# Optimization experiments

Measured on AMD Instinct MI355X. Metric: run time of the kernel, lower is better.

## Reference

```python
import jax, jax.numpy as jnp
import numpy as np

N_NODES = 50000
N_EDGES = 600000
IN_F = 128
HID_F = 128
OUT_F = 128


def setup_inputs() -> dict:
    key = jax.random.key(0)
    ks = jax.random.split(key, 12)
    features = jax.random.normal(ks[0], (N_NODES, IN_F), dtype=jnp.float32)
    src = jax.random.randint(ks[1], (N_EDGES,), 0, N_NODES, dtype=jnp.int32)
    dst = jax.random.randint(ks[2], (N_EDGES,), 0, N_NODES, dtype=jnp.int32)

    def lin(k, fan_in, fan_out):
        s = 1.0 / jnp.sqrt(fan_in)
        return jax.random.uniform(k, (fan_in, fan_out), jnp.float32, -s, s)

    return {
        "features": features, "src": src, "dst": dst,
        "W1_self": lin(ks[3], IN_F, HID_F), "W1_neigh": lin(ks[4], IN_F, HID_F),
        "b1": jnp.zeros((HID_F,), jnp.float32),
        "W2_self": lin(ks[5], HID_F, HID_F), "W2_neigh": lin(ks[6], HID_F, HID_F),
        "b2": jnp.zeros((HID_F,), jnp.float32),
        "W3_self": lin(ks[7], HID_F, OUT_F), "W3_neigh": lin(ks[8], HID_F, OUT_F),
        "b3": jnp.zeros((OUT_F,), jnp.float32),
    }


def _sage_mean(x, src, dst, W_self, W_neigh, b):
    # gather source-node features along edges, mean-reduce into dst nodes
    msgs = x[src]                                                # [E, d]
    summed = jax.ops.segment_sum(msgs, dst, num_segments=N_NODES)  # [N, d]
    deg = jax.ops.segment_sum(jnp.ones((dst.shape[0],), x.dtype), dst,
                              num_segments=N_NODES)               # [N]
    mean = summed / jnp.maximum(deg, 1.0)[:, None]
    return x @ W_self + mean @ W_neigh + b


def reference(features, src, dst,
              W1_self, W1_neigh, b1,
              W2_self, W2_neigh, b2,
              W3_self, W3_neigh, b3):
    x = features.reshape(features.shape[0], -1)  # Flatten (no-op for 2D)
    x = jax.nn.relu(_sage_mean(x, src, dst, W1_self, W1_neigh, b1))
    x = jax.nn.relu(_sage_mean(x, src, dst, W2_self, W2_neigh, b2))
    x = _sage_mean(x, src, dst, W3_self, W3_neigh, b3)
    return x
```

## Files before the change

### kernel.cpp

```cpp
#include <hip/hip_runtime.h>

#define NN 50000
#define NE 600000
#define F 128

typedef __attribute__((ext_vector_type(4))) float f4;
typedef __attribute__((ext_vector_type(4))) float f32x4;
typedef __bf16 bf16x8 __attribute__((ext_vector_type(8)));
typedef short short8v __attribute__((ext_vector_type(8)));
typedef unsigned short u16x8 __attribute__((ext_vector_type(8)));

__device__ inline ushort f2bf(float f) {
    uint u = __builtin_bit_cast(uint, f);
    uint r = (u + 0x7FFFu + ((u >> 16) & 1u)) >> 16;
    return (ushort)r;
}
__device__ inline float bf2f(ushort u) {
    uint t = ((uint)u) << 16;
    return __builtin_bit_cast(float, t);
}


__global__ void count_deg(const int* __restrict__ dst, int* __restrict__ deg, int E) {
    int e = blockIdx.x * blockDim.x + threadIdx.x;
    if (e < E) atomicAdd(&deg[dst[e]], 1);
}

__global__ __launch_bounds__(1024) void scan_part1(const int* __restrict__ deg,
                                                   int* __restrict__ bsum, int N) {
    __shared__ int ws[16];
    int tid = threadIdx.x;
    int idx = blockIdx.x * 1024 + tid;
    int v = (idx < N) ? deg[idx] : 0;
    #pragma unroll
    for (int o = 32; o; o >>= 1) v += __shfl_down(v, o);
    if ((tid & 63) == 0) ws[tid >> 6] = v;
    __syncthreads();
    if (tid < 64) {
        int t = (tid < 16) ? ws[tid] : 0;
        #pragma unroll
        for (int o = 8; o; o >>= 1) t += __shfl_down(t, o);
        if (tid == 0) bsum[blockIdx.x] = t;
    }
}

__global__ __launch_bounds__(1024) void scan_part3(const int* __restrict__ deg,
                                                   const int* __restrict__ bsum,
                                                   int* __restrict__ off,
                                                   int* __restrict__ cur,
                                                   float* __restrict__ recip,
                                                   int N, int NB) {
    __shared__ int wsum[16];
    __shared__ int sbase;
    int tid = threadIdx.x;
    int wid = tid >> 6;
    int lane = tid & 63;
    if (tid < 64) {
        int v = (tid < NB) ? bsum[tid] : 0;
        int x = v;
        #pragma unroll
        for (int o = 1; o < 64; o <<= 1) {
            int t = __shfl_up(x, o);
            if (lane >= o) x += t;
        }
        if (tid == blockIdx.x) sbase = x - v;
    }
    int idx = blockIdx.x * 1024 + tid;
    int v = (idx < N) ? deg[idx] : 0;
    int x = v;
    #pragma unroll
    for (int o = 1; o < 64; o <<= 1) {
        int t = __shfl_up(x, o);
        if (lane >= o) x += t;
    }
    if (lane == 63) wsum[wid] = x;
    __syncthreads();
    if (tid == 0) {
        int a = 0;
        #pragma unroll
        for (int w = 0; w < 16; ++w) { int t = wsum[w]; wsum[w] = a; a += t; }
    }
    __syncthreads();
    int incl = x + wsum[wid];
    if (idx < N) {
        int start = sbase + incl - v;
        off[idx] = start;
        cur[idx] = start;
        recip[idx] = 1.0f / (float)max(v, 1);
    }
}

__global__ void fill_csr(const int* __restrict__ src, const int* __restrict__ dst,
                         int* __restrict__ cur, int* __restrict__ csr, int E) {
    int e = blockIdx.x * blockDim.x + threadIdx.x;
    if (e < E) {
        int pos = atomicAdd(&cur[dst[e]], 1);
        csr[pos] = src[e];
    }
}


__global__ __launch_bounds__(256) void wt_prep(const float* __restrict__ W1s, const float* __restrict__ W1n,
                                               const float* __restrict__ W2s, const float* __restrict__ W2n,
                                               const float* __restrict__ W3s, const float* __restrict__ W3n,
                                               ushort* __restrict__ Bt1, ushort* __restrict__ Bt2,
                                               ushort* __restrict__ Bt3) {
    int layer = blockIdx.y;
    const float* Ws = (layer == 0) ? W1s : (layer == 1) ? W2s : W3s;
    const float* Wn = (layer == 0) ? W1n : (layer == 1) ? W2n : W3n;
    ushort* Bt = (layer == 0) ? Bt1 : (layer == 1) ? Bt2 : Bt3;
    int col = blockIdx.x;
    int k = threadIdx.x;
    float v = (k < 128) ? Ws[k * 128 + col] : Wn[(k - 128) * 128 + col];
    Bt[col * 256 + k] = f2bf(v);
}


__global__ __launch_bounds__(256) void to_bf16(const float* __restrict__ in,
                                               ushort* __restrict__ out, int n8) {
    int i = blockIdx.x * 256 + threadIdx.x;
    if (i < n8) {
        const f4* p = (const f4*)in + (size_t)i * 2;
        f4 a = p[0], b = p[1];
        short8v w;
        w[0] = (short)f2bf(a[0]); w[1] = (short)f2bf(a[1]);
        w[2] = (short)f2bf(a[2]); w[3] = (short)f2bf(a[3]);
        w[4] = (short)f2bf(b[0]); w[5] = (short)f2bf(b[1]);
        w[6] = (short)f2bf(b[2]); w[7] = (short)f2bf(b[3]);
        ((short8v*)out)[i] = w;
    }
}


template <int RELU, int OUTBF>
__global__ __launch_bounds__(256) void sage_layer(const ushort* __restrict__ xb,
                                                  const int* __restrict__ off,
                                                  const int* __restrict__ deg,
                                                  const float* __restrict__ recip,
                                                  const int* __restrict__ csr,
                                                  const ushort* __restrict__ Bt,
                                                  const float* __restrict__ bias,
                                                  void* __restrict__ outp, int N) {
    __shared__ ushort sa[32 * 256];
    int tid = threadIdx.x;
    int r0 = blockIdx.x * 32;

    {
        int row = tid >> 3;
        int c = tid & 7;
        int grow = r0 + row;
        uint sw = ((uint)row & 7u) << 4;
        uint base = (uint)(row * 512 + c * 32);
        short8v w0 = (short8v)0, w1 = (short8v)0;
        if (grow < N) {
            const short8v* sp = (const short8v*)&xb[(size_t)grow * 128 + c * 16];
            w0 = sp[0]; w1 = sp[1];
        }
        *(short8v*)((char*)sa + (base ^ sw)) = w0;
        *(short8v*)((char*)sa + ((base + 16) ^ sw)) = w1;
    }

    {
        int g = tid >> 4;
        int l16 = tid & 15;
        const ushort* xpb = xb + (size_t)l16 * 8;
        #pragma unroll
        for (int rep = 0; rep < 2; ++rep) {
            int row = g + rep * 16;
            int node = r0 + row;
            float a[8] = {0.f, 0.f, 0.f, 0.f, 0.f, 0.f, 0.f, 0.f};
            if (node < N) {
                int start = off[node];
                int d = deg[node];
                int nfull = d & ~7;
                int i = 0;
                for (; i < nfull; i += 8) {
                    int s[8];
                    #pragma unroll
                    for (int u = 0; u < 8; ++u) s[u] = csr[start + i + u];
                    u16x8 v[8];
                    #pragma unroll
                    for (int u = 0; u < 8; ++u) v[u] = *(const u16x8*)(xpb + (size_t)s[u] * 128);
                    #pragma unroll
                    for (int u = 0; u < 8; ++u) {
                        #pragma unroll
                        for (int j = 0; j < 8; ++j) a[j] += bf2f(v[u][j]);
                    }
                }
                if (i < d) {
                    int dm1 = d - 1;
                    int s[8];
                    #pragma unroll
                    for (int u = 0; u < 8; ++u) {
                        int idx = i + u;
                        s[u] = csr[start + ((idx < dm1) ? idx : dm1)];
                    }
                    u16x8 v[8];
                    #pragma unroll
                    for (int u = 0; u < 8; ++u) v[u] = *(const u16x8*)(xpb + (size_t)s[u] * 128);
                    #pragma unroll
                    for (int u = 0; u < 8; ++u) {
                        float m = (i + u < d) ? 1.f : 0.f;
                        #pragma unroll
                        for (int j = 0; j < 8; ++j) a[j] += m * bf2f(v[u][j]);
                    }
                }
                float r = recip[node];
                #pragma unroll
                for (int j = 0; j < 8; ++j) a[j] *= r;
            }
            short8v w;
            #pragma unroll
            for (int j = 0; j < 8; ++j) w[j] = (short)f2bf(a[j]);
            uint sw = ((uint)row & 7u) << 4;
            uint addr = (uint)(row * 512 + 256 + l16 * 16);
            *(short8v*)((char*)sa + (addr ^ sw)) = w;
        }
    }
    __syncthreads();

    int lane = tid & 63;
    int wid = tid >> 6;
    int wr = wid & 1;
    int wc = wid >> 1;
    int l15 = lane & 15;
    int lg = lane >> 4;

    int arow = wr * 16 + l15;
    uint abase = (uint)(arow * 512 + lg * 16);
    uint asw = ((uint)arow & 7u) << 4;
    bf16x8 a[8];
    #pragma unroll
    for (int ks = 0; ks < 8; ++ks) {
        a[ks] = *(const bf16x8*)((const char*)sa + ((abase + (uint)ks * 64) ^ asw));
    }

    f32x4 acc[4];
    #pragma unroll
    for (int ct = 0; ct < 4; ++ct) acc[ct] = (f32x4)0.f;

    #pragma unroll
    for (int ct = 0; ct < 4; ++ct) {
        int bcol = wc * 64 + ct * 16 + l15;
        const ushort* bp = Bt + bcol * 256 + lg * 8;
        #pragma unroll
        for (int ks = 0; ks < 8; ++ks) {
            bf16x8 b = *(const bf16x8*)(bp + ks * 32);
            acc[ct] = __builtin_amdgcn_mfma_f32_16x16x32_bf16(a[ks], b, acc[ct], 0, 0, 0);
        }
    }

    int crow = r0 + wr * 16 + lg * 4;
    #pragma unroll
    for (int ct = 0; ct < 4; ++ct) {
        int col = wc * 64 + ct * 16 + l15;
        float bv = bias[col];
        #pragma unroll
        for (int r = 0; r < 4; ++r) {
            int row = crow + r;
            if (row < N) {
                float v = acc[ct][r] + bv;
                if (RELU) v = fmaxf(v, 0.f);
                if (OUTBF) ((ushort*)outp)[(size_t)row * 128 + col] = f2bf(v);
                else       ((float*)outp)[(size_t)row * 128 + col] = v;
            }
        }
    }
}


extern "C" void kernel_launch(void* const* d_in, const int* in_sizes, int n_in,
                              void* d_out, int out_size, void* d_ws, size_t ws_size,
                              hipStream_t stream) {
    const float* feat = (const float*)d_in[0];
    const int* src = (const int*)d_in[1];
    const int* dst = (const int*)d_in[2];
    const float* W1s = (const float*)d_in[3];
    const float* W1n = (const float*)d_in[4];
    const float* b1 = (const float*)d_in[5];
    const float* W2s = (const float*)d_in[6];
    const float* W2n = (const float*)d_in[7];
    const float* b2 = (const float*)d_in[8];
    const float* W3s = (const float*)d_in[9];
    const float* W3n = (const float*)d_in[10];
    const float* b3 = (const float*)d_in[11];
    float* out = (float*)d_out;

    const int N = NN, E = NE;
    const int NB = (N + 1023) / 1024;

    char* p = (char*)d_ws;
    auto alloc = [&](size_t bytes) {
        char* q = p;
        p += (bytes + 255) & ~(size_t)255;
        return q;
    };
    int* deg = (int*)alloc((size_t)N * 4);
    int* off = (int*)alloc((size_t)N * 4);
    int* cur = (int*)alloc((size_t)N * 4);
    float* recip = (float*)alloc((size_t)N * 4);
    int* bsum = (int*)alloc(64 * 4);
    int* csr = (int*)alloc((size_t)E * 4);
    ushort* xb0 = (ushort*)alloc((size_t)N * F * 2);
    ushort* h1b = (ushort*)alloc((size_t)N * F * 2);
    ushort* h2b = (ushort*)alloc((size_t)N * F * 2);
    ushort* Bt1 = (ushort*)alloc(128 * 256 * 2);
    ushort* Bt2 = (ushort*)alloc(128 * 256 * 2);
    ushort* Bt3 = (ushort*)alloc(128 * 256 * 2);

    wt_prep<<<dim3(128, 3), 256, 0, stream>>>(W1s, W1n, W2s, W2n, W3s, W3n, Bt1, Bt2, Bt3);
    to_bf16<<<(N * F / 8 + 255) / 256, 256, 0, stream>>>(feat, xb0, N * F / 8);

    hipMemsetAsync(deg, 0, (size_t)N * 4, stream);
    count_deg<<<(E + 255) / 256, 256, 0, stream>>>(dst, deg, E);
    scan_part1<<<NB, 1024, 0, stream>>>(deg, bsum, N);
    scan_part3<<<NB, 1024, 0, stream>>>(deg, bsum, off, cur, recip, N, NB);
    fill_csr<<<(E + 255) / 256, 256, 0, stream>>>(src, dst, cur, csr, E);

    int grid = (N + 31) / 32;

    sage_layer<1, 1><<<grid, 256, 0, stream>>>(xb0, off, deg, recip, csr, Bt1, b1, h1b, N);
    sage_layer<1, 1><<<grid, 256, 0, stream>>>(h1b, off, deg, recip, csr, Bt2, b2, h2b, N);
    sage_layer<0, 0><<<grid, 256, 0, stream>>>(h2b, off, deg, recip, csr, Bt3, b3, out, N);
}
```

Measured before the change: 244.3 us.

## Halve rows per block and balance neighbor aggregation with shared atomic row queue

Each block now handles 16 node rows instead of 32, and the four 16-lane groups per wavefront pull rows dynamically from a shared atomic counter rather than being statically assigned two rows each. This is meant to even out work across groups when node degrees vary, and to give more blocks for occupancy and tail balance. The MFMA stage is re-split so each of the four waves computes 32 output columns over the 16 rows. The cost is an extra barrier and LDS atomics per row, a shuffle per row, and twice as many blocks, each reloading the weight matrix.

```diff
diff --git a/kernel.cpp b/kernel.cpp
--- a/kernel.cpp
+++ b/kernel.cpp
@@ -141,32 +141,34 @@
                                                   const ushort* __restrict__ Bt,
                                                   const float* __restrict__ bias,
                                                   void* __restrict__ outp, int N) {
-    __shared__ ushort sa[32 * 256];
+    __shared__ ushort sa[16 * 256];
+    __shared__ int wcnt;
     int tid = threadIdx.x;
-    int r0 = blockIdx.x * 32;
+    int r0 = blockIdx.x * 16;
+    if (tid == 0) wcnt = 0;
 
     {
-        int row = tid >> 3;
-        int c = tid & 7;
+        int row = tid >> 4;
+        int c = tid & 15;
         int grow = r0 + row;
         uint sw = ((uint)row & 7u) << 4;
-        uint base = (uint)(row * 512 + c * 32);
-        short8v w0 = (short8v)0, w1 = (short8v)0;
-        if (grow < N) {
-            const short8v* sp = (const short8v*)&xb[(size_t)grow * 128 + c * 16];
-            w0 = sp[0]; w1 = sp[1];
-        }
-        *(short8v*)((char*)sa + (base ^ sw)) = w0;
-        *(short8v*)((char*)sa + ((base + 16) ^ sw)) = w1;
-    }
+        uint base = (uint)(row * 512 + c * 16);
+        short8v w = (short8v)0;
+        if (grow < N) w = ((const short8v*)&xb[(size_t)grow * 128])[c];
+        *(short8v*)((char*)sa + (base ^ sw)) = w;
+    }
+    __syncthreads();
 
     {
-        int g = tid >> 4;
         int l16 = tid & 15;
+        int lanebase = (tid & 63) & ~15;
         const ushort* xpb = xb + (size_t)l16 * 8;
-        #pragma unroll
-        for (int rep = 0; rep < 2; ++rep) {
-            int row = g + rep * 16;
+        for (;;) {
+            int n = 0;
+            if (l16 == 0) n = atomicAdd(&wcnt, 1);
+            n = __shfl(n, lanebase);
+            if (n >= 16) break;
+            int row = n;
             int node = r0 + row;
             float a[8] = {0.f, 0.f, 0.f, 0.f, 0.f, 0.f, 0.f, 0.f};
             if (node < N) {
@@ -221,27 +223,24 @@
 
     int lane = tid & 63;
     int wid = tid >> 6;
-    int wr = wid & 1;
-    int wc = wid >> 1;
     int l15 = lane & 15;
     int lg = lane >> 4;
 
-    int arow = wr * 16 + l15;
-    uint abase = (uint)(arow * 512 + lg * 16);
-    uint asw = ((uint)arow & 7u) << 4;
+    uint abase = (uint)(l15 * 512 + lg * 16);
+    uint asw = ((uint)l15 & 7u) << 4;
     bf16x8 a[8];
     #pragma unroll
     for (int ks = 0; ks < 8; ++ks) {
         a[ks] = *(const bf16x8*)((const char*)sa + ((abase + (uint)ks * 64) ^ asw));
     }
 
-    f32x4 acc[4];
-    #pragma unroll
-    for (int ct = 0; ct < 4; ++ct) acc[ct] = (f32x4)0.f;
-
-    #pragma unroll
-    for (int ct = 0; ct < 4; ++ct) {
-        int bcol = wc * 64 + ct * 16 + l15;
+    f32x4 acc[2];
+    #pragma unroll
+    for (int ct = 0; ct < 2; ++ct) acc[ct] = (f32x4)0.f;
+
+    #pragma unroll
+    for (int ct = 0; ct < 2; ++ct) {
+        int bcol = wid * 32 + ct * 16 + l15;
         const ushort* bp = Bt + bcol * 256 + lg * 8;
         #pragma unroll
         for (int ks = 0; ks < 8; ++ks) {
@@ -250,10 +249,10 @@
         }
     }
 
-    int crow = r0 + wr * 16 + lg * 4;
-    #pragma unroll
-    for (int ct = 0; ct < 4; ++ct) {
-        int col = wc * 64 + ct * 16 + l15;
+    int crow = r0 + lg * 4;
+    #pragma unroll
+    for (int ct = 0; ct < 2; ++ct) {
+        int col = wid * 32 + ct * 16 + l15;
         float bv = bias[col];
         #pragma unroll
         for (int r = 0; r < 4; ++r) {
@@ -317,7 +316,7 @@
     scan_part3<<<NB, 1024, 0, stream>>>(deg, bsum, off, cur, recip, N, NB);
     fill_csr<<<(E + 255) / 256, 256, 0, stream>>>(src, dst, cur, csr, E);
 
-    int grid = (N + 31) / 32;
+    int grid = (N + 15) / 16;
 
     sage_layer<1, 1><<<grid, 256, 0, stream>>>(xb0, off, deg, recip, csr, Bt1, b1, h1b, N);
     sage_layer<1, 1><<<grid, 256, 0, stream>>>(h1b, off, deg, recip, csr, Bt2, b2, h2b, N);
```

Result: faster. 233.0 us, median of 2 (-4.6%).

## Dynamically assign aggregation rows via shared atomic counter and gather 16 neighbors per batch

Applied to the files above, without the earlier changes.

Replaces the static two-rows-per-16-lane-group assignment with a work queue: each 16-lane group grabs the next row index from a shared-memory atomic counter and broadcasts it by shuffle. This is meant to balance degree variance across groups within a block. It also merges the full and tail loops into one masked loop that issues 16 neighbor loads per iteration, raising memory-level parallelism. The cost is more registers, masked wasted loads for low-degree nodes (avg degree ~12), atomic traffic, and an added barrier.

```diff
diff --git a/kernel.cpp b/kernel.cpp
--- a/kernel.cpp
+++ b/kernel.cpp
@@ -142,8 +142,10 @@
                                                   const float* __restrict__ bias,
                                                   void* __restrict__ outp, int N) {
     __shared__ ushort sa[32 * 256];
+    __shared__ int wcnt;
     int tid = threadIdx.x;
     int r0 = blockIdx.x * 32;
+    if (tid == 0) wcnt = 0;
 
     {
         int row = tid >> 3;
@@ -159,48 +161,38 @@
         *(short8v*)((char*)sa + (base ^ sw)) = w0;
         *(short8v*)((char*)sa + ((base + 16) ^ sw)) = w1;
     }
+    __syncthreads();
 
     {
-        int g = tid >> 4;
         int l16 = tid & 15;
+        int lanebase = (tid & 63) & ~15;
         const ushort* xpb = xb + (size_t)l16 * 8;
-        #pragma unroll
-        for (int rep = 0; rep < 2; ++rep) {
-            int row = g + rep * 16;
+        for (;;) {
+            int n = 0;
+            if (l16 == 0) n = atomicAdd(&wcnt, 1);
+            n = __shfl(n, lanebase);
+            if (n >= 32) break;
+            int row = n;
             int node = r0 + row;
             float a[8] = {0.f, 0.f, 0.f, 0.f, 0.f, 0.f, 0.f, 0.f};
             if (node < N) {
                 int start = off[node];
                 int d = deg[node];
-                int nfull = d & ~7;
-                int i = 0;
-                for (; i < nfull; i += 8) {
-                    int s[8];
+                int dm1 = (d > 0) ? d - 1 : 0;
+                for (int i = 0; i < d; i += 16) {
+                    int rem = d - i;
+                    int s[16];
                     #pragma unroll
-                    for (int u = 0; u < 8; ++u) s[u] = csr[start + i + u];
-                    u16x8 v[8];
-                    #pragma unroll
-                    for (int u = 0; u < 8; ++u) v[u] = *(const u16x8*)(xpb + (size_t)s[u] * 128);
-                    #pragma unroll
-                    for (int u = 0; u < 8; ++u) {
-                        #pragma unroll
-                        for (int j = 0; j < 8; ++j) a[j] += bf2f(v[u][j]);
-                    }
-                }
-                if (i < d) {
-                    int dm1 = d - 1;
-                    int s[8];
-                    #pragma unroll
-                    for (int u = 0; u < 8; ++u) {
+                    for (int u = 0; u < 16; ++u) {
                         int idx = i + u;
                         s[u] = csr[start + ((idx < dm1) ? idx : dm1)];
                     }
-                    u16x8 v[8];
+                    u16x8 v[16];
                     #pragma unroll
-                    for (int u = 0; u < 8; ++u) v[u] = *(const u16x8*)(xpb + (size_t)s[u] * 128);
+                    for (int u = 0; u < 16; ++u) v[u] = *(const u16x8*)(xpb + (size_t)s[u] * 128);
                     #pragma unroll
-                    for (int u = 0; u < 8; ++u) {
-                        float m = (i + u < d) ? 1.f : 0.f;
+                    for (int u = 0; u < 16; ++u) {
+                        float m = (u < rem) ? 1.f : 0.f;
                         #pragma unroll
                         for (int j = 0; j < 8; ++j) a[j] += m * bf2f(v[u][j]);
                     }
```

Result: slower. 275.1 us (+12.6%).

## Transform-then-aggregate: GEMM before neighbor mean, split into gemm and agg kernels

Applied to the files above, without the earlier changes.

Reorders each SAGE layer to compute x@W_self+b and x@W_neigh first in a GEMM kernel, then aggregates the projected neighbor features with a separate gather-and-add kernel that applies the mean, residual sum and ReLU. This splits the fused gather+GEMM kernel into two launches per layer. The gather size is unchanged since the dims are equal, but it adds round trips through two extra N x 128 bf16 buffers and extra launches. It also adds another bf16 rounding point before aggregation.

```diff
diff --git a/kernel.cpp b/kernel.cpp
--- a/kernel.cpp
+++ b/kernel.cpp
@@ -100,7 +100,7 @@
 }
 
 
-__global__ __launch_bounds__(256) void wt_prep(const float* __restrict__ W1s, const float* __restrict__ W1n,
+__global__ __launch_bounds__(128) void wt_prep(const float* __restrict__ W1s, const float* __restrict__ W1n,
                                                const float* __restrict__ W2s, const float* __restrict__ W2n,
                                                const float* __restrict__ W3s, const float* __restrict__ W3n,
                                                ushort* __restrict__ Bt1, ushort* __restrict__ Bt2,
@@ -111,8 +111,8 @@
     ushort* Bt = (layer == 0) ? Bt1 : (layer == 1) ? Bt2 : Bt3;
     int col = blockIdx.x;
     int k = threadIdx.x;
-    float v = (k < 128) ? Ws[k * 128 + col] : Wn[(k - 128) * 128 + col];
-    Bt[col * 256 + k] = f2bf(v);
+    float v = (col < 128) ? Ws[k * 128 + col] : Wn[k * 128 + (col - 128)];
+    Bt[col * 128 + k] = f2bf(v);
 }
 
 
@@ -132,16 +132,12 @@
 }
 
 
-template <int RELU, int OUTBF>
-__global__ __launch_bounds__(256) void sage_layer(const ushort* __restrict__ xb,
-                                                  const int* __restrict__ off,
-                                                  const int* __restrict__ deg,
-                                                  const float* __restrict__ recip,
-                                                  const int* __restrict__ csr,
-                                                  const ushort* __restrict__ Bt,
-                                                  const float* __restrict__ bias,
-                                                  void* __restrict__ outp, int N) {
-    __shared__ ushort sa[32 * 256];
+__global__ __launch_bounds__(256) void gemm2(const ushort* __restrict__ xb,
+                                             const ushort* __restrict__ Bt,
+                                             const float* __restrict__ bias,
+                                             ushort* __restrict__ y,
+                                             ushort* __restrict__ z, int N) {
+    __shared__ ushort sa[32 * 128];
     int tid = threadIdx.x;
     int r0 = blockIdx.x * 32;
 
@@ -150,7 +146,7 @@
         int c = tid & 7;
         int grow = r0 + row;
         uint sw = ((uint)row & 7u) << 4;
-        uint base = (uint)(row * 512 + c * 32);
+        uint base = (uint)(row * 256 + c * 32);
         short8v w0 = (short8v)0, w1 = (short8v)0;
         if (grow < N) {
             const short8v* sp = (const short8v*)&xb[(size_t)grow * 128 + c * 16];
@@ -158,64 +154,6 @@
         }
         *(short8v*)((char*)sa + (base ^ sw)) = w0;
         *(short8v*)((char*)sa + ((base + 16) ^ sw)) = w1;
-    }
-
-    {
-        int g = tid >> 4;
-        int l16 = tid & 15;
-        const ushort* xpb = xb + (size_t)l16 * 8;
-        #pragma unroll
-        for (int rep = 0; rep < 2; ++rep) {
-            int row = g + rep * 16;
-            int node = r0 + row;
-            float a[8] = {0.f, 0.f, 0.f, 0.f, 0.f, 0.f, 0.f, 0.f};
-            if (node < N) {
-                int start = off[node];
-                int d = deg[node];
-                int nfull = d & ~7;
-                int i = 0;
-                for (; i < nfull; i += 8) {
-                    int s[8];
-                    #pragma unroll
-                    for (int u = 0; u < 8; ++u) s[u] = csr[start + i + u];
-                    u16x8 v[8];
-                    #pragma unroll
-                    for (int u = 0; u < 8; ++u) v[u] = *(const u16x8*)(xpb + (size_t)s[u] * 128);
-                    #pragma unroll
-                    for (int u = 0; u < 8; ++u) {
-                        #pragma unroll
-                        for (int j = 0; j < 8; ++j) a[j] += bf2f(v[u][j]);
-                    }
-                }
-                if (i < d) {
-                    int dm1 = d - 1;
-                    int s[8];
-                    #pragma unroll
-                    for (int u = 0; u < 8; ++u) {
-                        int idx = i + u;
-                        s[u] = csr[start + ((idx < dm1) ? idx : dm1)];
-                    }
-                    u16x8 v[8];
-                    #pragma unroll
-                    for (int u = 0; u < 8; ++u) v[u] = *(const u16x8*)(xpb + (size_t)s[u] * 128);
-                    #pragma unroll
-                    for (int u = 0; u < 8; ++u) {
-                        float m = (i + u < d) ? 1.f : 0.f;
-                        #pragma unroll
-                        for (int j = 0; j < 8; ++j) a[j] += m * bf2f(v[u][j]);
-                    }
-                }
-                float r = recip[node];
-                #pragma unroll
-                for (int j = 0; j < 8; ++j) a[j] *= r;
-            }
-            short8v w;
-            #pragma unroll
-            for (int j = 0; j < 8; ++j) w[j] = (short)f2bf(a[j]);
-            uint sw = ((uint)row & 7u) << 4;
-            uint addr = (uint)(row * 512 + 256 + l16 * 16);
-            *(short8v*)((char*)sa + (addr ^ sw)) = w;
-        }
     }
     __syncthreads();
 
@@ -227,24 +165,24 @@
     int lg = lane >> 4;
 
     int arow = wr * 16 + l15;
-    uint abase = (uint)(arow * 512 + lg * 16);
+    uint abase = (uint)(arow * 256 + lg * 16);
     uint asw = ((uint)arow & 7u) << 4;
-    bf16x8 a[8];
-    #pragma unroll
-    for (int ks = 0; ks < 8; ++ks) {
+    bf16x8 a[4];
+    #pragma unroll
+    for (int ks = 0; ks < 4; ++ks) {
         a[ks] = *(const bf16x8*)((const char*)sa + ((abase + (uint)ks * 64) ^ asw));
     }
 
-    f32x4 acc[4];
-    #pragma unroll
-    for (int ct = 0; ct < 4; ++ct) acc[ct] = (f32x4)0.f;
-
-    #pragma unroll
-    for (int ct = 0; ct < 4; ++ct) {
-        int bcol = wc * 64 + ct * 16 + l15;
-        const ushort* bp = Bt + bcol * 256 + lg * 8;
-        #pragma unroll
-        for (int ks = 0; ks < 8; ++ks) {
+    f32x4 acc[8];
+    #pragma unroll
+    for (int ct = 0; ct < 8; ++ct) acc[ct] = (f32x4)0.f;
+
+    #pragma unroll
+    for (int ct = 0; ct < 8; ++ct) {
+        int bcol = wc * 128 + ct * 16 + l15;
+        const ushort* bp = Bt + bcol * 128 + lg * 8;
+        #pragma unroll
+        for (int ks = 0; ks < 4; ++ks) {
             bf16x8 b = *(const bf16x8*)(bp + ks * 32);
             acc[ct] = __builtin_amdgcn_mfma_f32_16x16x32_bf16(a[ks], b, acc[ct], 0, 0, 0);
         }
@@ -252,19 +190,87 @@
 
     int crow = r0 + wr * 16 + lg * 4;
     #pragma unroll
-    for (int ct = 0; ct < 4; ++ct) {
-        int col = wc * 64 + ct * 16 + l15;
-        float bv = bias[col];
+    for (int ct = 0; ct < 8; ++ct) {
+        int col = wc * 128 + ct * 16 + l15;
+        float bv = (col < 128) ? bias[col] : 0.f;
+        ushort* dst = (col < 128) ? (y + col) : (z + col - 128);
         #pragma unroll
         for (int r = 0; r < 4; ++r) {
             int row = crow + r;
-            if (row < N) {
-                float v = acc[ct][r] + bv;
-                if (RELU) v = fmaxf(v, 0.f);
-                if (OUTBF) ((ushort*)outp)[(size_t)row * 128 + col] = f2bf(v);
-                else       ((float*)outp)[(size_t)row * 128 + col] = v;
-            }
-        }
+            if (row < N) dst[(size_t)row * 128] = f2bf(acc[ct][r] + bv);
+        }
+    }
+}
+
+
+template <int RELU, int OUTBF>
+__global__ __launch_bounds__(256) void agg_add(const ushort* __restrict__ y,
+                                               const ushort* __restrict__ z,
+                                               const int* __restrict__ off,
+                                               const int* __restrict__ deg,
+                                               const float* __restrict__ recip,
+                                               const int* __restrict__ csr,
+                                               void* __restrict__ outp, int N) {
+    int node = blockIdx.x * 16 + (threadIdx.x >> 4);
+    if (node >= N) return;
+    int l16 = threadIdx.x & 15;
+    const ushort* zpb = z + (size_t)l16 * 8;
+    float a[8] = {0.f, 0.f, 0.f, 0.f, 0.f, 0.f, 0.f, 0.f};
+    int start = off[node];
+    int d = deg[node];
+    int nfull = d & ~7;
+    int i = 0;
+    for (; i < nfull; i += 8) {
+        int s[8];
+        #pragma unroll
+        for (int u = 0; u < 8; ++u) s[u] = csr[start + i + u];
+        u16x8 v[8];
+        #pragma unroll
+        for (int u = 0; u < 8; ++u) v[u] = *(const u16x8*)(zpb + (size_t)s[u] * 128);
+        #pragma unroll
+        for (int u = 0; u < 8; ++u) {
+            #pragma unroll
+            for (int j = 0; j < 8; ++j) a[j] += bf2f(v[u][j]);
+        }
+    }
+    if (i < d) {
+        int dm1 = d - 1;
+        int s[8];
+        #pragma unroll
+        for (int u = 0; u < 8; ++u) {
+            int idx = i + u;
+            s[u] = csr[start + ((idx < dm1) ? idx : dm1)];
+        }
+        u16x8 v[8];
+        #pragma unroll
+        for (int u = 0; u < 8; ++u) v[u] = *(const u16x8*)(zpb + (size_t)s[u] * 128);
+        #pragma unroll
+        for (int u = 0; u < 8; ++u) {
+            float m = (i + u < d) ? 1.f : 0.f;
+            #pragma unroll
+            for (int j = 0; j < 8; ++j) a[j] += m * bf2f(v[u][j]);
+        }
+    }
+    float r = recip[node];
+    u16x8 yv = *(const u16x8*)(y + (size_t)node * 128 + l16 * 8);
+    float o[8];
+    #pragma unroll
+    for (int j = 0; j < 8; ++j) {
+        o[j] = bf2f(yv[j]) + a[j] * r;
+        if (RELU) o[j] = fmaxf(o[j], 0.f);
+    }
+    if (OUTBF) {
+        u16x8 w;
+        #pragma unroll
+        for (int j = 0; j < 8; ++j) w[j] = f2bf(o[j]);
+        *(u16x8*)((ushort*)outp + (size_t)node * 128 + l16 * 8) = w;
+    } else {
+        float* op = (float*)outp + (size_t)node * 128 + l16 * 8;
+        f4 w0, w1;
+        w0[0] = o[0]; w0[1] = o[1]; w0[2] = o[2]; w0[3] = o[3];
+        w1[0] = o[4]; w1[1] = o[5]; w1[2] = o[6]; w1[3] = o[7];
+        *(f4*)op = w0;
+        *(f4*)(op + 4) = w1;
     }
 }
 
@@ -304,11 +310,13 @@
     ushort* xb0 = (ushort*)alloc((size_t)N * F * 2);
     ushort* h1b = (ushort*)alloc((size_t)N * F * 2);
     ushort* h2b = (ushort*)alloc((size_t)N * F * 2);
-    ushort* Bt1 = (ushort*)alloc(128 * 256 * 2);
-    ushort* Bt2 = (ushort*)alloc(128 * 256 * 2);
-    ushort* Bt3 = (ushort*)alloc(128 * 256 * 2);
-
-    wt_prep<<<dim3(128, 3), 256, 0, stream>>>(W1s, W1n, W2s, W2n, W3s, W3n, Bt1, Bt2, Bt3);
+    ushort* ybuf = (ushort*)alloc((size_t)N * F * 2);
+    ushort* zbuf = (ushort*)alloc((size_t)N * F * 2);
+    ushort* Bt1 = (ushort*)alloc(256 * 128 * 2);
+    ushort* Bt2 = (ushort*)alloc(256 * 128 * 2);
+    ushort* Bt3 = (ushort*)alloc(256 * 128 * 2);
+
+    wt_prep<<<dim3(256, 3), 128, 0, stream>>>(W1s, W1n, W2s, W2n, W3s, W3n, Bt1, Bt2, Bt3);
     to_bf16<<<(N * F / 8 + 255) / 256, 256, 0, stream>>>(feat, xb0, N * F / 8);
 
     hipMemsetAsync(deg, 0, (size_t)N * 4, stream);
@@ -317,9 +325,13 @@
     scan_part3<<<NB, 1024, 0, stream>>>(deg, bsum, off, cur, recip, N, NB);
     fill_csr<<<(E + 255) / 256, 256, 0, stream>>>(src, dst, cur, csr, E);
 
-    int grid = (N + 31) / 32;
-
-    sage_layer<1, 1><<<grid, 256, 0, stream>>>(xb0, off, deg, recip, csr, Bt1, b1, h1b, N);
-    sage_layer<1, 1><<<grid, 256, 0, stream>>>(h1b, off, deg, recip, csr, Bt2, b2, h2b, N);
-    sage_layer<0, 0><<<grid, 256, 0, stream>>>(h2b, off, deg, recip, csr, Bt3, b3, out, N);
-}
+    int ggrid = (N + 31) / 32;
+    int agrid = (N + 15) / 16;
+
+    gemm2<<<ggrid, 256, 0, stream>>>(xb0, Bt1, b1, ybuf, zbuf, N);
+    agg_add<1, 1><<<agrid, 256, 0, stream>>>(ybuf, zbuf, off, deg, recip, csr, h1b, N);
+    gemm2<<<ggrid, 256, 0, stream>>>(h1b, Bt2, b2, ybuf, zbuf, N);
+    agg_add<1, 1><<<agrid, 256, 0, stream>>>(ybuf, zbuf, off, deg, recip, csr, h2b, N);
+    gemm2<<<ggrid, 256, 0, stream>>>(h2b, Bt3, b3, ybuf, zbuf, N);
+    agg_add<0, 0><<<agrid, 256, 0, stream>>>(ybuf, zbuf, off, deg, recip, csr, out, N);
+}
```

Result: slower. 276.8 us (+13.3%).
